# Optimization experiments

Hardware: AMD Instinct MI355X
Metric: run time of the kernel (lower is better)

The kernel has to match this reference:

```python
import jax, jax.numpy as jnp
import numpy as np
import math

D_MODEL = 1024
NUM_HEADS = 16
D_K = D_MODEL // NUM_HEADS
B, S = 2, 2048


def setup_inputs() -> dict:
    key = jax.random.key(0)
    ks = jax.random.split(key, 11)
    scale = 1.0 / math.sqrt(D_MODEL)
    inp = {
        "query": jax.random.normal(ks[0], (B, S, D_MODEL), jnp.float32),
        "key": jax.random.normal(ks[1], (B, S, D_MODEL), jnp.float32),
        "value": jax.random.normal(ks[2], (B, S, D_MODEL), jnp.float32),
        "Wq": jax.random.normal(ks[3], (D_MODEL, D_MODEL), jnp.float32) * scale,
        "bq": jnp.zeros((D_MODEL,), jnp.float32),
        "Wk": jax.random.normal(ks[4], (D_MODEL, D_MODEL), jnp.float32) * scale,
        "bk": jnp.zeros((D_MODEL,), jnp.float32),
        "Wv": jax.random.normal(ks[5], (D_MODEL, D_MODEL), jnp.float32) * scale,
        "bv": jnp.zeros((D_MODEL,), jnp.float32),
        "Wo": jax.random.normal(ks[6], (D_MODEL, D_MODEL), jnp.float32) * scale,
        "bo": jnp.zeros((D_MODEL,), jnp.float32),
    }
    return inp


def reference(query, key, value, Wq, bq, Wk, bk, Wv, bv, Wo, bo):
    b, s, _ = query.shape
    # QKV projections (torch Linear: x @ W.T + b)
    Q = query @ Wq.T + bq
    K = key @ Wk.T + bk
    V = value @ Wv.T + bv
    # [b, h, s, d_k]
    Q = Q.reshape(b, s, NUM_HEADS, D_K).transpose(0, 2, 1, 3)
    K = K.reshape(b, s, NUM_HEADS, D_K).transpose(0, 2, 1, 3)
    V = V.reshape(b, s, NUM_HEADS, D_K).transpose(0, 2, 1, 3)
    score = jnp.einsum("bhqd,bhkd->bhqk", Q, K) / math.sqrt(D_K)
    attn = jax.nn.softmax(score, axis=-1)
    out = jnp.einsum("bhqk,bhkd->bhqd", attn, V)
    out = out.transpose(0, 2, 1, 3).reshape(b, s, D_MODEL)
    return out @ Wo.T + bo
```

## Files before the change

kernel.cpp:

```cpp
#include <hip/hip_runtime.h>

#define NHEADS 16
#define SEQ    2048
#define BATCH  2
#define DMODEL 1024
#define MTOT   4096

typedef __attribute__((ext_vector_type(8)))  short short8;
typedef __attribute__((ext_vector_type(4)))  float f32x4;
typedef __attribute__((ext_vector_type(16))) float f32x16;

__device__ __forceinline__ unsigned short f32_to_bf16_rn(float x) {
  unsigned int u = __float_as_uint(x);
  u += 0x7fffu + ((u >> 16) & 1u);
  return (unsigned short)(u >> 16);
}

__device__ __forceinline__ unsigned cvt_pk_bf16(float lo, float hi_) {
  unsigned r;
  asm("v_cvt_pk_bf16_f32 %0, %1, %2" : "=v"(r) : "v"(lo), "v"(hi_));
  return r;
}

__device__ __forceinline__ void permlane32_swap(unsigned &a, unsigned &b) {
  asm("v_permlane32_swap_b32 %0, %1" : "+v"(a), "+v"(b));
}

__device__ __forceinline__ void async16(void* lds, const void* g) {
  __builtin_amdgcn_global_load_lds((const __attribute__((address_space(1))) unsigned int*)g,
                                   (__attribute__((address_space(3))) unsigned int*)lds, 16, 0, 0);
}

__global__ void cvt_bf16_kernel(const float* __restrict__ x0, const float* __restrict__ x1,
                                const float* __restrict__ x2,
                                const float* __restrict__ w0, const float* __restrict__ w1,
                                const float* __restrict__ w2, const float* __restrict__ w3,
                                unsigned short* __restrict__ obase)
{
  const int e = (blockIdx.x*256 + threadIdx.x)*8;
  const float* src;
  int local;
  if (e < 3*4194304) {
    const int t = e >> 22;
    src = t==0 ? x0 : t==1 ? x1 : x2;
    local = e & (4194304-1);
    src += local;
    local += t << 22;
  } else {
    const int f = e - 3*4194304;
    const int t = f >> 20;
    src = t==0 ? w0 : t==1 ? w1 : t==2 ? w2 : w3;
    src += (f & (1048576-1));
    local = e;
  }
  const float4 v0 = *(const float4*)(src);
  const float4 v1 = *(const float4*)(src + 4);
  union { unsigned short u[8]; uint4 v; } r;
  r.u[0] = f32_to_bf16_rn(v0.x); r.u[1] = f32_to_bf16_rn(v0.y);
  r.u[2] = f32_to_bf16_rn(v0.z); r.u[3] = f32_to_bf16_rn(v0.w);
  r.u[4] = f32_to_bf16_rn(v1.x); r.u[5] = f32_to_bf16_rn(v1.y);
  r.u[6] = f32_to_bf16_rn(v1.z); r.u[7] = f32_to_bf16_rn(v1.w);
  *(uint4*)(obase + local) = r.v;
}

template<int BM>
__device__ __forceinline__ void gemm_core(const unsigned short* __restrict__ A,
                                          const unsigned short* __restrict__ W,
                                          unsigned short* sA, unsigned short* sB,
                                          int m0, int n0, f32x4 (&acc)[BM/32][4])
{
  constexpr int MI = BM/32;
  const int t = threadIdx.x;
  const int lane = t & 63;
  const int wv = t >> 6;
  const int wm = wv >> 1, wn = wv & 1;
  const int lr = lane & 15, lk = lane >> 4;

  for (int kt = 0; kt < DMODEL/64; ++kt) {
    #pragma unroll
    for (int g = 0; g < MI; ++g) {
      const int o  = g*4096 + t*16;
      const int so = o ^ (((o >> 7) & 7) << 4);
      const int row = so >> 7, colE = (so & 127) >> 1;
      async16((char*)sA + o, A + (size_t)(m0 + row)*DMODEL + kt*64 + colE);
    }
    #pragma unroll
    for (int g = 0; g < 4; ++g) {
      const int o  = g*4096 + t*16;
      const int so = o ^ (((o >> 7) & 7) << 4);
      const int row = so >> 7, colE = (so & 127) >> 1;
      async16((char*)sB + o, W + (size_t)(n0 + row)*DMODEL + kt*64 + colE);
    }
    __syncthreads();
    #pragma unroll
    for (int ks = 0; ks < 2; ++ks) {
      short8 af[MI], bf[4];
      #pragma unroll
      for (int mi = 0; mi < MI; ++mi) {
        const int row = wm*(BM/2) + mi*16 + lr;
        const int sl  = (ks*4 + lk) ^ (row & 7);
        af[mi] = *(const short8*)(sA + row*64 + sl*8);
      }
      #pragma unroll
      for (int ni = 0; ni < 4; ++ni) {
        const int row = wn*64 + ni*16 + lr;
        const int sl  = (ks*4 + lk) ^ (row & 7);
        bf[ni] = *(const short8*)(sB + row*64 + sl*8);
      }
      #pragma unroll
      for (int mi = 0; mi < MI; ++mi)
        #pragma unroll
        for (int ni = 0; ni < 4; ++ni)
          acc[mi][ni] = __builtin_amdgcn_mfma_f32_16x16x32_bf16(af[mi], bf[ni], acc[mi][ni], 0, 0, 0);
    }
    __syncthreads();
  }
}

__global__ __launch_bounds__(256, 3)
void qkv_gemm_kernel(const unsigned short* __restrict__ Xq, const unsigned short* __restrict__ Xk,
                     const unsigned short* __restrict__ Xv,
                     const unsigned short* __restrict__ Wq, const unsigned short* __restrict__ Wk,
                     const unsigned short* __restrict__ Wv,
                     const float* __restrict__ bq, const float* __restrict__ bk,
                     const float* __restrict__ bv,
                     unsigned short* __restrict__ Qp, unsigned short* __restrict__ Kp,
                     unsigned short* __restrict__ Vtp)
{
  constexpr int BM = 128;
  constexpr int MI = BM/32;
  __shared__ __align__(16) unsigned short smem[17024];
  unsigned short* sA = smem;
  unsigned short* sB = smem + 8192;

  const int m0   = blockIdx.x * BM;
  const int nabs = blockIdx.y * 128;
  const int wsel = nabs >> 10;
  const int n0   = nabs & 1023;
  const unsigned short* A = wsel==0 ? Xq : wsel==1 ? Xk : Xv;
  const unsigned short* W = wsel==0 ? Wq : wsel==1 ? Wk : Wv;
  const float* bias       = wsel==0 ? bq : wsel==1 ? bk : bv;

  f32x4 acc[MI][4];
  #pragma unroll
  for (int mi = 0; mi < MI; ++mi)
    #pragma unroll
    for (int ni = 0; ni < 4; ++ni)
      acc[mi][ni] = {0.f, 0.f, 0.f, 0.f};

  gemm_core<BM>(A, W, sA, sB, m0, n0, acc);

  const int t = threadIdx.x, lane = t & 63, wvx = t >> 6;
  const int wm = wvx >> 1, wn = wvx & 1;
  const int lr = lane & 15, lk = lane >> 4;

  if (wsel == 2) {
    #pragma unroll
    for (int ni = 0; ni < 4; ++ni) {
      const float badd = bias[n0 + wn*64 + ni*16 + lr];
      #pragma unroll
      for (int mi = 0; mi < MI; ++mi)
        #pragma unroll
        for (int r = 0; r < 4; ++r) {
          const int ml = wm*(BM/2) + mi*16 + lk*4 + r;
          smem[(wn*64 + ni*16 + lr)*132 + ml] = f32_to_bf16_rn(acc[mi][ni][r] + badd);
        }
    }
    __syncthreads();
    const int bb = m0 >> 11, s0 = m0 & 2047;
    const int jr = (t & 15)*8, nr = t >> 4;
    #pragma unroll
    for (int pass = 0; pass < 8; ++pass) {
      const int n  = pass*16 + nr;
      const int nn = n0 + n, hh = nn >> 6, d = nn & 63;
      const short8 v = *(const short8*)(smem + n*132 + jr);
      *(short8*)(Vtp + (((size_t)bb*NHEADS + hh)*64 + d)*SEQ + s0 + jr) = v;
    }
  } else {
    unsigned short* dst = wsel==0 ? Qp : Kp;
    const float qscale = (wsel == 0) ? 0.125f * 1.4426950408889634f : 1.0f;
    #pragma unroll
    for (int ni = 0; ni < 4; ++ni) {
      const int nn = n0 + wn*64 + ni*16 + lr;
      const float badd = bias[nn];
      const int hh = nn >> 6, d = nn & 63;
      #pragma unroll
      for (int mi = 0; mi < MI; ++mi) {
        #pragma unroll
        for (int r = 0; r < 4; ++r) {
          const int m = m0 + wm*(BM/2) + mi*16 + lk*4 + r;
          const int bb = m >> 11, s = m & 2047;
          const float v = (acc[mi][ni][r] + badd) * qscale;
          dst[(((size_t)bb*NHEADS + hh)*SEQ + s)*64 + d] = f32_to_bf16_rn(v);
        }
      }
    }
  }
}

__global__ __launch_bounds__(256, 4)
void attn_kernel(const unsigned short* __restrict__ Qp, const unsigned short* __restrict__ Kp,
                 const unsigned short* __restrict__ Vtp,
                 unsigned short* __restrict__ Opar, float* __restrict__ Lpar)
{
  __shared__ __align__(16) unsigned short sm[16384];
  constexpr int NT = 1024/64;

  const int t = threadIdx.x, lane = t & 63, w = t >> 6;
  const int lq = lane & 31, hi = lane >> 5;
  const int f   = blockIdx.x;
  const int wid = (f & 7)*128 + (f >> 3);
  const int qt = wid & 15, h = (wid >> 4) & 15, b = (wid >> 8) & 1, half = wid >> 9;

  const size_t bh = (size_t)b*NHEADS + h;
  const unsigned short* Qh = Qp  + bh*SEQ*64;
  const unsigned short* Kh = Kp  + bh*SEQ*64 + (size_t)half*1024*64;
  const unsigned short* Vh = Vtp + bh*64*SEQ;
  const int q0 = qt*128 + w*32;

  const int stag = f & 3;
  for (int i = 0; i < stag; ++i) {
    __builtin_amdgcn_s_sleep(15);
    __builtin_amdgcn_s_sleep(15);
  }

  short8 qf[4];
  #pragma unroll
  for (int ks = 0; ks < 4; ++ks)
    qf[ks] = *(const short8*)(Qh + (size_t)(q0 + lq)*64 + ks*16 + hi*8);

  const unsigned short* srcp0;
  size_t sstride;
  if (w < 2) { srcp0 = Kh + (size_t)(w*32 + lq)*64 + hi*8;                      sstride = 64*64; }
  else       { srcp0 = Vh + (size_t)((w-2)*32 + lq)*2048 + half*1024 + hi*8;    sstride = 64;    }

  #pragma unroll
  for (int i = 0; i < 4; ++i)
    async16((char*)sm + w*4096 + i*1024, srcp0 + i*16);

  f32x16 o[2];
  float lsa[4] = {0.f, 0.f, 0.f, 0.f};
  #pragma unroll
  for (int d = 0; d < 2; ++d)
    #pragma unroll
    for (int r = 0; r < 16; ++r) o[d][r] = 0.f;

  #pragma unroll 2
  for (int kt = 0; kt < NT; ++kt) {
    {
      const unsigned short* sp = srcp0 + (size_t)((kt + 1) & (NT - 1))*sstride;
      const int nb = ((kt + 1) & 1) * 16384;
      #pragma unroll
      for (int i = 0; i < 4; ++i)
        async16((char*)sm + nb + w*4096 + i*1024, sp + i*16);
    }
    asm volatile("s_waitcnt vmcnt(4)" ::: "memory");
    __builtin_amdgcn_s_barrier();

    const unsigned short* base  = sm + (kt & 1)*8192;
    const unsigned short* vbase = base + 4096;

    f32x16 st[2];
    #pragma unroll
    for (int s = 0; s < 2; ++s)
      #pragma unroll
      for (int r = 0; r < 16; ++r) st[s][r] = 0.f;
    __builtin_amdgcn_s_setprio(1);
    #pragma unroll
    for (int sub = 0; sub < 2; ++sub)
      #pragma unroll
      for (int ks = 0; ks < 4; ++ks) {
        const short8 kf = *(const short8*)(base + (sub*4 + ks)*512 + lane*8);
        st[sub] = __builtin_amdgcn_mfma_f32_32x32x16_bf16(kf, qf[ks], st[sub], 0, 0, 0);
      }
    __builtin_amdgcn_s_setprio(0);

    #pragma unroll
    for (int s = 0; s < 2; ++s)
      #pragma unroll
      for (int r = 0; r < 16; ++r) {
        const float p = __builtin_amdgcn_exp2f(st[s][r]);
        st[s][r] = p;
        lsa[r & 3] += p;
      }

    #pragma unroll
    for (int sub = 0; sub < 2; ++sub) {
      union { unsigned u[4]; short8 s; } pA, pB;
      {
        unsigned x0 = cvt_pk_bf16(st[sub][0],  st[sub][1]);
        unsigned x1 = cvt_pk_bf16(st[sub][2],  st[sub][3]);
        unsigned y0 = cvt_pk_bf16(st[sub][4],  st[sub][5]);
        unsigned y1 = cvt_pk_bf16(st[sub][6],  st[sub][7]);
        permlane32_swap(x0, y0);
        permlane32_swap(x1, y1);
        pA.u[0] = x0; pA.u[1] = x1; pA.u[2] = y0; pA.u[3] = y1;
        unsigned z0 = cvt_pk_bf16(st[sub][8],  st[sub][9]);
        unsigned z1 = cvt_pk_bf16(st[sub][10], st[sub][11]);
        unsigned w0 = cvt_pk_bf16(st[sub][12], st[sub][13]);
        unsigned w1 = cvt_pk_bf16(st[sub][14], st[sub][15]);
        permlane32_swap(z0, w0);
        permlane32_swap(z1, w1);
        pB.u[0] = z0; pB.u[1] = z1; pB.u[2] = w0; pB.u[3] = w1;
      }
      const short8 v00 = *(const short8*)(vbase + (0*4 + 2*sub    )*512 + lane*8);
      const short8 v01 = *(const short8*)(vbase + (0*4 + 2*sub + 1)*512 + lane*8);
      const short8 v10 = *(const short8*)(vbase + (1*4 + 2*sub    )*512 + lane*8);
      const short8 v11 = *(const short8*)(vbase + (1*4 + 2*sub + 1)*512 + lane*8);
      __builtin_amdgcn_s_setprio(1);
      o[0] = __builtin_amdgcn_mfma_f32_32x32x16_bf16(v00, pA.s, o[0], 0, 0, 0);
      o[1] = __builtin_amdgcn_mfma_f32_32x32x16_bf16(v10, pA.s, o[1], 0, 0, 0);
      o[0] = __builtin_amdgcn_mfma_f32_32x32x16_bf16(v01, pB.s, o[0], 0, 0, 0);
      o[1] = __builtin_amdgcn_mfma_f32_32x32x16_bf16(v11, pB.s, o[1], 0, 0, 0);
      __builtin_amdgcn_s_setprio(0);
    }
    asm volatile("" ::: "memory");
    __builtin_amdgcn_s_barrier();
  }

  float lsum = (lsa[0] + lsa[1]) + (lsa[2] + lsa[3]);
  lsum += __shfl_xor(lsum, 32);
  if (lane < 32)
    Lpar[half*65536 + b*32768 + h*2048 + q0 + lq] = lsum;

  const size_t row = (size_t)b*SEQ + q0 + lq;
  unsigned short* orow = Opar + ((size_t)half*MTOT + row)*DMODEL + h*64;
  #pragma unroll
  for (int dblk = 0; dblk < 2; ++dblk)
    #pragma unroll
    for (int g = 0; g < 4; ++g) {
      union { unsigned short us[4]; uint2 v; } pk;
      #pragma unroll
      for (int r = 0; r < 4; ++r) pk.us[r] = f32_to_bf16_rn(o[dblk][g*4 + r]);
      *(uint2*)(orow + dblk*32 + g*8 + hi*4) = pk.v;
    }
}

__global__ void combine_kernel(const unsigned short* __restrict__ Opar,
                               const float* __restrict__ Lpar,
                               unsigned short* __restrict__ Op)
{
  const int flat = blockIdx.x*256 + threadIdx.x;
  const int row  = flat >> 8;
  const int col4 = flat & 255;
  const int b = row >> 11, q = row & 2047, h = col4 >> 4;

  const uint2 a = *(const uint2*)(Opar + (size_t)row*DMODEL + col4*4);
  const uint2 c = *(const uint2*)(Opar + (size_t)(MTOT + row)*DMODEL + col4*4);
  const float l0 = Lpar[b*32768 + h*2048 + q];
  const float l1 = Lpar[65536 + b*32768 + h*2048 + q];
  const float inv = __builtin_amdgcn_rcpf(l0 + l1);

  union { unsigned u[2]; uint2 v; } ua, uc;
  ua.v = a; uc.v = c;
  union { unsigned short us[4]; uint2 v; } out;
  #pragma unroll
  for (int j = 0; j < 4; ++j) {
    const unsigned va = ((j & 1) ? (ua.u[j >> 1] >> 16) : (ua.u[j >> 1] & 0xffffu)) << 16;
    const unsigned vc = ((j & 1) ? (uc.u[j >> 1] >> 16) : (uc.u[j >> 1] & 0xffffu)) << 16;
    const float s = (__uint_as_float(va) + __uint_as_float(vc)) * inv;
    out.us[j] = f32_to_bf16_rn(s);
  }
  *(uint2*)(Op + (size_t)row*DMODEL + col4*4) = out.v;
}

__global__ __launch_bounds__(256, 2)
void oproj_gemm_kernel(const unsigned short* __restrict__ Oin, const unsigned short* __restrict__ Wo,
                       const float* __restrict__ bo, float* __restrict__ out)
{
  constexpr int BM = 64;
  constexpr int MI = BM/32;
  __shared__ __align__(16) unsigned short sA[BM*64];
  __shared__ __align__(16) unsigned short sB[128*64];
  const int m0 = blockIdx.x * BM;
  const int n0 = blockIdx.y * 128;

  f32x4 acc[MI][4];
  #pragma unroll
  for (int mi = 0; mi < MI; ++mi)
    #pragma unroll
    for (int ni = 0; ni < 4; ++ni)
      acc[mi][ni] = {0.f,0.f,0.f,0.f};

  gemm_core<BM>(Oin, Wo, sA, sB, m0, n0, acc);

  const int t = threadIdx.x, lane = t & 63, wvx = t >> 6;
  const int wm = wvx >> 1, wn = wvx & 1;
  const int lr = lane & 15, lk = lane >> 4;

  #pragma unroll
  for (int ni = 0; ni < 4; ++ni) {
    const int nn = n0 + wn*64 + ni*16 + lr;
    const float badd = bo[nn];
    #pragma unroll
    for (int mi = 0; mi < MI; ++mi)
      #pragma unroll
      for (int r = 0; r < 4; ++r) {
        const int m = m0 + wm*(BM/2) + mi*16 + lk*4 + r;
        out[(size_t)m*DMODEL + nn] = acc[mi][ni][r] + badd;
      }
  }
}

extern "C" void kernel_launch(void* const* d_in, const int* in_sizes, int n_in,
                              void* d_out, int out_size, void* d_ws, size_t ws_size,
                              hipStream_t stream) {
  const float* query = (const float*)d_in[0];
  const float* key   = (const float*)d_in[1];
  const float* value = (const float*)d_in[2];
  const float* Wq    = (const float*)d_in[3];
  const float* bq    = (const float*)d_in[4];
  const float* Wk    = (const float*)d_in[5];
  const float* bk    = (const float*)d_in[6];
  const float* Wv    = (const float*)d_in[7];
  const float* bv    = (const float*)d_in[8];
  const float* Wo    = (const float*)d_in[9];
  const float* bo    = (const float*)d_in[10];

  const size_t NX = (size_t)MTOT*DMODEL;
  const size_t NW = (size_t)DMODEL*DMODEL;
  unsigned short* w   = (unsigned short*)d_ws;
  unsigned short* Xq  = w;
  unsigned short* Xk  = Xq  + NX;
  unsigned short* Xv  = Xk  + NX;
  unsigned short* Wqp = Xv  + NX;
  unsigned short* Wkp = Wqp + NW;
  unsigned short* Wvp = Wkp + NW;
  unsigned short* Wop = Wvp + NW;
  unsigned short* Qp  = Wop + NW;
  unsigned short* Kp  = Qp  + NX;
  unsigned short* Vtp = Kp  + NX;
  unsigned short* Opb = Vtp + NX;
  unsigned short* Opar = w;
  float*          Lpar = (float*)(w + 2*NX);

  cvt_bf16_kernel<<<dim3(8192), 256, 0, stream>>>(
      query, key, value, Wq, Wk, Wv, Wo, w);
  qkv_gemm_kernel<<<dim3(32, 24), 256, 0, stream>>>(
      Xq, Xk, Xv, Wqp, Wkp, Wvp, bq, bk, bv, Qp, Kp, Vtp);
  attn_kernel<<<dim3(1024), 256, 0, stream>>>(Qp, Kp, Vtp, Opar, Lpar);
  combine_kernel<<<dim3(4096), 256, 0, stream>>>(Opar, Lpar, Opb);
  oproj_gemm_kernel<<<dim3(64, 8), 256, 0, stream>>>(Opb, Wop, bo, (float*)d_out);
}
```

Baseline: 122.5 us.

## Process two 32-row query sub-tiles per wave to reuse K/V LDS tiles

Each wave now handles 64 query rows (two 32-row halves) instead of 32, so every K and V fragment read from LDS feeds two MFMAs. The grid is halved to 512 blocks, launch bounds drop to 2 blocks per CU, and the s_sleep start stagger and the zeroing of score accumulators are removed (the first MFMA now takes a zero input). This cuts LDS traffic and global K/V loads per unit of work, at the cost of more registers, lower occupancy and fewer blocks to spread across CUs.

```diff
diff --git a/kernel.cpp b/kernel.cpp
--- a/kernel.cpp
+++ b/kernel.cpp
@@ -198,7 +198,7 @@
   }
 }
 
-__global__ __launch_bounds__(256, 4)
+__global__ __launch_bounds__(256, 2)
 void attn_kernel(const unsigned short* __restrict__ Qp, const unsigned short* __restrict__ Kp,
                  const unsigned short* __restrict__ Vtp,
                  unsigned short* __restrict__ Opar, float* __restrict__ Lpar)
@@ -209,25 +209,25 @@
   const int t = threadIdx.x, lane = t & 63, w = t >> 6;
   const int lq = lane & 31, hi = lane >> 5;
   const int f   = blockIdx.x;
-  const int wid = (f & 7)*128 + (f >> 3);
-  const int qt = wid & 15, h = (wid >> 4) & 15, b = (wid >> 8) & 1, half = wid >> 9;
+  const int wid = (f & 7)*64 + (f >> 3);
+  const int qt = wid & 7, h = (wid >> 3) & 15, b = (wid >> 7) & 1, half = (wid >> 8) & 1;
 
   const size_t bh = (size_t)b*NHEADS + h;
   const unsigned short* Qh = Qp  + bh*SEQ*64;
   const unsigned short* Kh = Kp  + bh*SEQ*64 + (size_t)half*1024*64;
   const unsigned short* Vh = Vtp + bh*64*SEQ;
-  const int q0 = qt*128 + w*32;
-
-  const int stag = f & 3;
-  for (int i = 0; i < stag; ++i) {
-    __builtin_amdgcn_s_sleep(15);
-    __builtin_amdgcn_s_sleep(15);
-  }
-
-  short8 qf[4];
-  #pragma unroll
-  for (int ks = 0; ks < 4; ++ks)
-    qf[ks] = *(const short8*)(Qh + (size_t)(q0 + lq)*64 + ks*16 + hi*8);
+  const int q0 = qt*256 + w*64;
+
+  short8 qf[2][4];
+  #pragma unroll
+  for (int qh = 0; qh < 2; ++qh)
+    #pragma unroll
+    for (int ks = 0; ks < 4; ++ks)
+      qf[qh][ks] = *(const short8*)(Qh + (size_t)(q0 + qh*32 + lq)*64 + ks*16 + hi*8);
+
+  f32x16 z16;
+  #pragma unroll
+  for (int r = 0; r < 16; ++r) z16[r] = 0.f;
 
   const unsigned short* srcp0;
   size_t sstride;
@@ -238,14 +238,18 @@
   for (int i = 0; i < 4; ++i)
     async16((char*)sm + w*4096 + i*1024, srcp0 + i*16);
 
-  f32x16 o[2];
-  float lsa[4] = {0.f, 0.f, 0.f, 0.f};
-  #pragma unroll
-  for (int d = 0; d < 2; ++d)
-    #pragma unroll
-    for (int r = 0; r < 16; ++r) o[d][r] = 0.f;
-
-  #pragma unroll 2
+  f32x16 o[2][2];
+  float lsa[2][4];
+  #pragma unroll
+  for (int qh = 0; qh < 2; ++qh) {
+    #pragma unroll
+    for (int d = 0; d < 2; ++d)
+      #pragma unroll
+      for (int r = 0; r < 16; ++r) o[qh][d][r] = 0.f;
+    #pragma unroll
+    for (int j = 0; j < 4; ++j) lsa[qh][j] = 0.f;
+  }
+
   for (int kt = 0; kt < NT; ++kt) {
     {
       const unsigned short* sp = srcp0 + (size_t)((kt + 1) & (NT - 1))*sstride;
@@ -260,80 +264,101 @@
     const unsigned short* base  = sm + (kt & 1)*8192;
     const unsigned short* vbase = base + 4096;
 
-    f32x16 st[2];
-    #pragma unroll
-    for (int s = 0; s < 2; ++s)
-      #pragma unroll
-      for (int r = 0; r < 16; ++r) st[s][r] = 0.f;
+    f32x16 st[2][2];
     __builtin_amdgcn_s_setprio(1);
     #pragma unroll
-    for (int sub = 0; sub < 2; ++sub)
+    for (int sub = 0; sub < 2; ++sub) {
       #pragma unroll
       for (int ks = 0; ks < 4; ++ks) {
         const short8 kf = *(const short8*)(base + (sub*4 + ks)*512 + lane*8);
-        st[sub] = __builtin_amdgcn_mfma_f32_32x32x16_bf16(kf, qf[ks], st[sub], 0, 0, 0);
-      }
+        if (ks == 0) {
+          st[0][sub] = __builtin_amdgcn_mfma_f32_32x32x16_bf16(kf, qf[0][0], z16, 0, 0, 0);
+          st[1][sub] = __builtin_amdgcn_mfma_f32_32x32x16_bf16(kf, qf[1][0], z16, 0, 0, 0);
+        } else {
+          st[0][sub] = __builtin_amdgcn_mfma_f32_32x32x16_bf16(kf, qf[0][ks], st[0][sub], 0, 0, 0);
+          st[1][sub] = __builtin_amdgcn_mfma_f32_32x32x16_bf16(kf, qf[1][ks], st[1][sub], 0, 0, 0);
+        }
+      }
+    }
     __builtin_amdgcn_s_setprio(0);
 
-    #pragma unroll
-    for (int s = 0; s < 2; ++s)
-      #pragma unroll
-      for (int r = 0; r < 16; ++r) {
-        const float p = __builtin_amdgcn_exp2f(st[s][r]);
-        st[s][r] = p;
-        lsa[r & 3] += p;
-      }
-
-    #pragma unroll
-    for (int sub = 0; sub < 2; ++sub) {
-      union { unsigned u[4]; short8 s; } pA, pB;
-      {
-        unsigned x0 = cvt_pk_bf16(st[sub][0],  st[sub][1]);
-        unsigned x1 = cvt_pk_bf16(st[sub][2],  st[sub][3]);
-        unsigned y0 = cvt_pk_bf16(st[sub][4],  st[sub][5]);
-        unsigned y1 = cvt_pk_bf16(st[sub][6],  st[sub][7]);
+    unsigned pw[2][2][8];
+    #pragma unroll
+    for (int qh = 0; qh < 2; ++qh)
+      #pragma unroll
+      for (int sub = 0; sub < 2; ++sub) {
+        #pragma unroll
+        for (int r = 0; r < 16; ++r) {
+          const float p = __builtin_amdgcn_exp2f(st[qh][sub][r]);
+          st[qh][sub][r] = p;
+          lsa[qh][r & 3] += p;
+        }
+        unsigned x0 = cvt_pk_bf16(st[qh][sub][0],  st[qh][sub][1]);
+        unsigned x1 = cvt_pk_bf16(st[qh][sub][2],  st[qh][sub][3]);
+        unsigned y0 = cvt_pk_bf16(st[qh][sub][4],  st[qh][sub][5]);
+        unsigned y1 = cvt_pk_bf16(st[qh][sub][6],  st[qh][sub][7]);
         permlane32_swap(x0, y0);
         permlane32_swap(x1, y1);
-        pA.u[0] = x0; pA.u[1] = x1; pA.u[2] = y0; pA.u[3] = y1;
-        unsigned z0 = cvt_pk_bf16(st[sub][8],  st[sub][9]);
-        unsigned z1 = cvt_pk_bf16(st[sub][10], st[sub][11]);
-        unsigned w0 = cvt_pk_bf16(st[sub][12], st[sub][13]);
-        unsigned w1 = cvt_pk_bf16(st[sub][14], st[sub][15]);
+        pw[qh][sub][0] = x0; pw[qh][sub][1] = x1; pw[qh][sub][2] = y0; pw[qh][sub][3] = y1;
+        unsigned z0 = cvt_pk_bf16(st[qh][sub][8],  st[qh][sub][9]);
+        unsigned z1 = cvt_pk_bf16(st[qh][sub][10], st[qh][sub][11]);
+        unsigned w0 = cvt_pk_bf16(st[qh][sub][12], st[qh][sub][13]);
+        unsigned w1 = cvt_pk_bf16(st[qh][sub][14], st[qh][sub][15]);
         permlane32_swap(z0, w0);
         permlane32_swap(z1, w1);
-        pB.u[0] = z0; pB.u[1] = z1; pB.u[2] = w0; pB.u[3] = w1;
-      }
+        pw[qh][sub][4] = z0; pw[qh][sub][5] = z1; pw[qh][sub][6] = w0; pw[qh][sub][7] = w1;
+      }
+
+    #pragma unroll
+    for (int sub = 0; sub < 2; ++sub) {
       const short8 v00 = *(const short8*)(vbase + (0*4 + 2*sub    )*512 + lane*8);
       const short8 v01 = *(const short8*)(vbase + (0*4 + 2*sub + 1)*512 + lane*8);
       const short8 v10 = *(const short8*)(vbase + (1*4 + 2*sub    )*512 + lane*8);
       const short8 v11 = *(const short8*)(vbase + (1*4 + 2*sub + 1)*512 + lane*8);
       __builtin_amdgcn_s_setprio(1);
-      o[0] = __builtin_amdgcn_mfma_f32_32x32x16_bf16(v00, pA.s, o[0], 0, 0, 0);
-      o[1] = __builtin_amdgcn_mfma_f32_32x32x16_bf16(v10, pA.s, o[1], 0, 0, 0);
-      o[0] = __builtin_amdgcn_mfma_f32_32x32x16_bf16(v01, pB.s, o[0], 0, 0, 0);
-      o[1] = __builtin_amdgcn_mfma_f32_32x32x16_bf16(v11, pB.s, o[1], 0, 0, 0);
+      #pragma unroll
+      for (int qh = 0; qh < 2; ++qh) {
+        union { unsigned u[4]; short8 s; } pA, pB;
+        pA.u[0] = pw[qh][sub][0]; pA.u[1] = pw[qh][sub][1];
+        pA.u[2] = pw[qh][sub][2]; pA.u[3] = pw[qh][sub][3];
+        pB.u[0] = pw[qh][sub][4]; pB.u[1] = pw[qh][sub][5];
+        pB.u[2] = pw[qh][sub][6]; pB.u[3] = pw[qh][sub][7];
+        o[qh][0] = __builtin_amdgcn_mfma_f32_32x32x16_bf16(v00, pA.s, o[qh][0], 0, 0, 0);
+        o[qh][1] = __builtin_amdgcn_mfma_f32_32x32x16_bf16(v10, pA.s, o[qh][1], 0, 0, 0);
+        o[qh][0] = __builtin_amdgcn_mfma_f32_32x32x16_bf16(v01, pB.s, o[qh][0], 0, 0, 0);
+        o[qh][1] = __builtin_amdgcn_mfma_f32_32x32x16_bf16(v11, pB.s, o[qh][1], 0, 0, 0);
+      }
       __builtin_amdgcn_s_setprio(0);
     }
     asm volatile("" ::: "memory");
     __builtin_amdgcn_s_barrier();
   }
 
-  float lsum = (lsa[0] + lsa[1]) + (lsa[2] + lsa[3]);
-  lsum += __shfl_xor(lsum, 32);
-  if (lane < 32)
-    Lpar[half*65536 + b*32768 + h*2048 + q0 + lq] = lsum;
-
-  const size_t row = (size_t)b*SEQ + q0 + lq;
-  unsigned short* orow = Opar + ((size_t)half*MTOT + row)*DMODEL + h*64;
-  #pragma unroll
-  for (int dblk = 0; dblk < 2; ++dblk)
-    #pragma unroll
-    for (int g = 0; g < 4; ++g) {
-      union { unsigned short us[4]; uint2 v; } pk;
-      #pragma unroll
-      for (int r = 0; r < 4; ++r) pk.us[r] = f32_to_bf16_rn(o[dblk][g*4 + r]);
-      *(uint2*)(orow + dblk*32 + g*8 + hi*4) = pk.v;
-    }
+  float lsum[2];
+  #pragma unroll
+  for (int qh = 0; qh < 2; ++qh) {
+    lsum[qh] = (lsa[qh][0] + lsa[qh][1]) + (lsa[qh][2] + lsa[qh][3]);
+    lsum[qh] += __shfl_xor(lsum[qh], 32);
+  }
+  if (lane < 32) {
+    Lpar[half*65536 + b*32768 + h*2048 + q0 + lq]      = lsum[0];
+    Lpar[half*65536 + b*32768 + h*2048 + q0 + 32 + lq] = lsum[1];
+  }
+
+  #pragma unroll
+  for (int qh = 0; qh < 2; ++qh) {
+    const size_t row = (size_t)b*SEQ + q0 + qh*32 + lq;
+    unsigned short* orow = Opar + ((size_t)half*MTOT + row)*DMODEL + h*64;
+    #pragma unroll
+    for (int dblk = 0; dblk < 2; ++dblk)
+      #pragma unroll
+      for (int g = 0; g < 4; ++g) {
+        union { unsigned short us[4]; uint2 v; } pk;
+        #pragma unroll
+        for (int r = 0; r < 4; ++r) pk.us[r] = f32_to_bf16_rn(o[qh][dblk][g*4 + r]);
+        *(uint2*)(orow + dblk*32 + g*8 + hi*4) = pk.v;
+      }
+  }
 }
 
 __global__ void combine_kernel(const unsigned short* __restrict__ Opar,
@@ -438,7 +463,7 @@
       query, key, value, Wq, Wk, Wv, Wo, w);
   qkv_gemm_kernel<<<dim3(32, 24), 256, 0, stream>>>(
       Xq, Xk, Xv, Wqp, Wkp, Wvp, bq, bk, bv, Qp, Kp, Vtp);
-  attn_kernel<<<dim3(1024), 256, 0, stream>>>(Qp, Kp, Vtp, Opar, Lpar);
+  attn_kernel<<<dim3(512), 256, 0, stream>>>(Qp, Kp, Vtp, Opar, Lpar);
   combine_kernel<<<dim3(4096), 256, 0, stream>>>(Opar, Lpar, Opb);
   oproj_gemm_kernel<<<dim3(64, 8), 256, 0, stream>>>(Opb, Wop, bo, (float*)d_out);
 }
```

Measured after the change: 118.1 us. 3.6% less time.

## Drop split-KV attention and combine kernel; each block processes full key range

Applied to the files above, without the earlier changes.

Removes the two-way key split in the attention kernel so each block iterates over all 2048 keys and normalizes its output directly, eliminating the separate combine kernel and the partial output/sum buffers. The grid halves to 512 blocks and launch bounds drop to 2 blocks per SM. It also removes the startup sleep staggering and the setprio hints, zero-initializes the score MFMA via a constant zero operand, and groups the exp/convert work before the PV MFMAs. The trade is fewer blocks (less parallelism and latency hiding) against saving a kernel launch plus the partial-result memory traffic.

```diff
diff --git a/kernel.cpp b/kernel.cpp
--- a/kernel.cpp
+++ b/kernel.cpp
@@ -198,41 +198,38 @@
   }
 }
 
-__global__ __launch_bounds__(256, 4)
+__global__ __launch_bounds__(256, 2)
 void attn_kernel(const unsigned short* __restrict__ Qp, const unsigned short* __restrict__ Kp,
-                 const unsigned short* __restrict__ Vtp,
-                 unsigned short* __restrict__ Opar, float* __restrict__ Lpar)
+                 const unsigned short* __restrict__ Vtp, unsigned short* __restrict__ Op)
 {
   __shared__ __align__(16) unsigned short sm[16384];
-  constexpr int NT = 1024/64;
+  constexpr int NT = SEQ/64;
 
   const int t = threadIdx.x, lane = t & 63, w = t >> 6;
   const int lq = lane & 31, hi = lane >> 5;
   const int f   = blockIdx.x;
-  const int wid = (f & 7)*128 + (f >> 3);
-  const int qt = wid & 15, h = (wid >> 4) & 15, b = (wid >> 8) & 1, half = wid >> 9;
+  const int wid = (f & 7)*64 + (f >> 3);
+  const int qt = wid & 15, h = (wid >> 4) & 15, b = wid >> 8;
 
   const size_t bh = (size_t)b*NHEADS + h;
   const unsigned short* Qh = Qp  + bh*SEQ*64;
-  const unsigned short* Kh = Kp  + bh*SEQ*64 + (size_t)half*1024*64;
+  const unsigned short* Kh = Kp  + bh*SEQ*64;
   const unsigned short* Vh = Vtp + bh*64*SEQ;
   const int q0 = qt*128 + w*32;
 
-  const int stag = f & 3;
-  for (int i = 0; i < stag; ++i) {
-    __builtin_amdgcn_s_sleep(15);
-    __builtin_amdgcn_s_sleep(15);
-  }
-
   short8 qf[4];
   #pragma unroll
   for (int ks = 0; ks < 4; ++ks)
     qf[ks] = *(const short8*)(Qh + (size_t)(q0 + lq)*64 + ks*16 + hi*8);
 
+  f32x16 z16;
+  #pragma unroll
+  for (int r = 0; r < 16; ++r) z16[r] = 0.f;
+
   const unsigned short* srcp0;
   size_t sstride;
-  if (w < 2) { srcp0 = Kh + (size_t)(w*32 + lq)*64 + hi*8;                      sstride = 64*64; }
-  else       { srcp0 = Vh + (size_t)((w-2)*32 + lq)*2048 + half*1024 + hi*8;    sstride = 64;    }
+  if (w < 2) { srcp0 = Kh + (size_t)(w*32 + lq)*64 + hi*8;       sstride = 64*64; }
+  else       { srcp0 = Vh + (size_t)((w-2)*32 + lq)*2048 + hi*8; sstride = 64;    }
 
   #pragma unroll
   for (int i = 0; i < 4; ++i)
@@ -245,7 +242,6 @@
     #pragma unroll
     for (int r = 0; r < 16; ++r) o[d][r] = 0.f;
 
-  #pragma unroll 2
   for (int kt = 0; kt < NT; ++kt) {
     {
       const unsigned short* sp = srcp0 + (size_t)((kt + 1) & (NT - 1))*sstride;
@@ -262,57 +258,55 @@
 
     f32x16 st[2];
     #pragma unroll
-    for (int s = 0; s < 2; ++s)
-      #pragma unroll
-      for (int r = 0; r < 16; ++r) st[s][r] = 0.f;
-    __builtin_amdgcn_s_setprio(1);
-    #pragma unroll
-    for (int sub = 0; sub < 2; ++sub)
+    for (int sub = 0; sub < 2; ++sub) {
       #pragma unroll
       for (int ks = 0; ks < 4; ++ks) {
         const short8 kf = *(const short8*)(base + (sub*4 + ks)*512 + lane*8);
-        st[sub] = __builtin_amdgcn_mfma_f32_32x32x16_bf16(kf, qf[ks], st[sub], 0, 0, 0);
-      }
-    __builtin_amdgcn_s_setprio(0);
-
-    #pragma unroll
-    for (int s = 0; s < 2; ++s)
+        if (ks == 0)
+          st[sub] = __builtin_amdgcn_mfma_f32_32x32x16_bf16(kf, qf[0], z16, 0, 0, 0);
+        else
+          st[sub] = __builtin_amdgcn_mfma_f32_32x32x16_bf16(kf, qf[ks], st[sub], 0, 0, 0);
+      }
+    }
+
+    unsigned pw[2][8];
+    #pragma unroll
+    for (int sub = 0; sub < 2; ++sub) {
       #pragma unroll
       for (int r = 0; r < 16; ++r) {
-        const float p = __builtin_amdgcn_exp2f(st[s][r]);
-        st[s][r] = p;
+        const float p = __builtin_amdgcn_exp2f(st[sub][r]);
+        st[sub][r] = p;
         lsa[r & 3] += p;
       }
+      unsigned x0 = cvt_pk_bf16(st[sub][0],  st[sub][1]);
+      unsigned x1 = cvt_pk_bf16(st[sub][2],  st[sub][3]);
+      unsigned y0 = cvt_pk_bf16(st[sub][4],  st[sub][5]);
+      unsigned y1 = cvt_pk_bf16(st[sub][6],  st[sub][7]);
+      permlane32_swap(x0, y0);
+      permlane32_swap(x1, y1);
+      pw[sub][0] = x0; pw[sub][1] = x1; pw[sub][2] = y0; pw[sub][3] = y1;
+      unsigned z0 = cvt_pk_bf16(st[sub][8],  st[sub][9]);
+      unsigned z1 = cvt_pk_bf16(st[sub][10], st[sub][11]);
+      unsigned w0 = cvt_pk_bf16(st[sub][12], st[sub][13]);
+      unsigned w1 = cvt_pk_bf16(st[sub][14], st[sub][15]);
+      permlane32_swap(z0, w0);
+      permlane32_swap(z1, w1);
+      pw[sub][4] = z0; pw[sub][5] = z1; pw[sub][6] = w0; pw[sub][7] = w1;
+    }
 
     #pragma unroll
     for (int sub = 0; sub < 2; ++sub) {
-      union { unsigned u[4]; short8 s; } pA, pB;
-      {
-        unsigned x0 = cvt_pk_bf16(st[sub][0],  st[sub][1]);
-        unsigned x1 = cvt_pk_bf16(st[sub][2],  st[sub][3]);
-        unsigned y0 = cvt_pk_bf16(st[sub][4],  st[sub][5]);
-        unsigned y1 = cvt_pk_bf16(st[sub][6],  st[sub][7]);
-        permlane32_swap(x0, y0);
-        permlane32_swap(x1, y1);
-        pA.u[0] = x0; pA.u[1] = x1; pA.u[2] = y0; pA.u[3] = y1;
-        unsigned z0 = cvt_pk_bf16(st[sub][8],  st[sub][9]);
-        unsigned z1 = cvt_pk_bf16(st[sub][10], st[sub][11]);
-        unsigned w0 = cvt_pk_bf16(st[sub][12], st[sub][13]);
-        unsigned w1 = cvt_pk_bf16(st[sub][14], st[sub][15]);
-        permlane32_swap(z0, w0);
-        permlane32_swap(z1, w1);
-        pB.u[0] = z0; pB.u[1] = z1; pB.u[2] = w0; pB.u[3] = w1;
-      }
       const short8 v00 = *(const short8*)(vbase + (0*4 + 2*sub    )*512 + lane*8);
       const short8 v01 = *(const short8*)(vbase + (0*4 + 2*sub + 1)*512 + lane*8);
       const short8 v10 = *(const short8*)(vbase + (1*4 + 2*sub    )*512 + lane*8);
       const short8 v11 = *(const short8*)(vbase + (1*4 + 2*sub + 1)*512 + lane*8);
-      __builtin_amdgcn_s_setprio(1);
+      union { unsigned u[4]; short8 s; } pA, pB;
+      pA.u[0] = pw[sub][0]; pA.u[1] = pw[sub][1]; pA.u[2] = pw[sub][2]; pA.u[3] = pw[sub][3];
+      pB.u[0] = pw[sub][4]; pB.u[1] = pw[sub][5]; pB.u[2] = pw[sub][6]; pB.u[3] = pw[sub][7];
       o[0] = __builtin_amdgcn_mfma_f32_32x32x16_bf16(v00, pA.s, o[0], 0, 0, 0);
       o[1] = __builtin_amdgcn_mfma_f32_32x32x16_bf16(v10, pA.s, o[1], 0, 0, 0);
       o[0] = __builtin_amdgcn_mfma_f32_32x32x16_bf16(v01, pB.s, o[0], 0, 0, 0);
       o[1] = __builtin_amdgcn_mfma_f32_32x32x16_bf16(v11, pB.s, o[1], 0, 0, 0);
-      __builtin_amdgcn_s_setprio(0);
     }
     asm volatile("" ::: "memory");
     __builtin_amdgcn_s_barrier();
@@ -320,48 +314,17 @@
 
   float lsum = (lsa[0] + lsa[1]) + (lsa[2] + lsa[3]);
   lsum += __shfl_xor(lsum, 32);
-  if (lane < 32)
-    Lpar[half*65536 + b*32768 + h*2048 + q0 + lq] = lsum;
-
-  const size_t row = (size_t)b*SEQ + q0 + lq;
-  unsigned short* orow = Opar + ((size_t)half*MTOT + row)*DMODEL + h*64;
+  const float inv = __builtin_amdgcn_rcpf(lsum);
+  unsigned short* orow = Op + ((size_t)b*SEQ + q0 + lq)*DMODEL + h*64;
   #pragma unroll
   for (int dblk = 0; dblk < 2; ++dblk)
     #pragma unroll
     for (int g = 0; g < 4; ++g) {
       union { unsigned short us[4]; uint2 v; } pk;
       #pragma unroll
-      for (int r = 0; r < 4; ++r) pk.us[r] = f32_to_bf16_rn(o[dblk][g*4 + r]);
+      for (int r = 0; r < 4; ++r) pk.us[r] = f32_to_bf16_rn(o[dblk][g*4 + r] * inv);
       *(uint2*)(orow + dblk*32 + g*8 + hi*4) = pk.v;
     }
-}
-
-__global__ void combine_kernel(const unsigned short* __restrict__ Opar,
-                               const float* __restrict__ Lpar,
-                               unsigned short* __restrict__ Op)
-{
-  const int flat = blockIdx.x*256 + threadIdx.x;
-  const int row  = flat >> 8;
-  const int col4 = flat & 255;
-  const int b = row >> 11, q = row & 2047, h = col4 >> 4;
-
-  const uint2 a = *(const uint2*)(Opar + (size_t)row*DMODEL + col4*4);
-  const uint2 c = *(const uint2*)(Opar + (size_t)(MTOT + row)*DMODEL + col4*4);
-  const float l0 = Lpar[b*32768 + h*2048 + q];
-  const float l1 = Lpar[65536 + b*32768 + h*2048 + q];
-  const float inv = __builtin_amdgcn_rcpf(l0 + l1);
-
-  union { unsigned u[2]; uint2 v; } ua, uc;
-  ua.v = a; uc.v = c;
-  union { unsigned short us[4]; uint2 v; } out;
-  #pragma unroll
-  for (int j = 0; j < 4; ++j) {
-    const unsigned va = ((j & 1) ? (ua.u[j >> 1] >> 16) : (ua.u[j >> 1] & 0xffffu)) << 16;
-    const unsigned vc = ((j & 1) ? (uc.u[j >> 1] >> 16) : (uc.u[j >> 1] & 0xffffu)) << 16;
-    const float s = (__uint_as_float(va) + __uint_as_float(vc)) * inv;
-    out.us[j] = f32_to_bf16_rn(s);
-  }
-  *(uint2*)(Op + (size_t)row*DMODEL + col4*4) = out.v;
 }
 
 __global__ __launch_bounds__(256, 2)
@@ -431,14 +394,11 @@
   unsigned short* Kp  = Qp  + NX;
   unsigned short* Vtp = Kp  + NX;
   unsigned short* Opb = Vtp + NX;
-  unsigned short* Opar = w;
-  float*          Lpar = (float*)(w + 2*NX);
 
   cvt_bf16_kernel<<<dim3(8192), 256, 0, stream>>>(
       query, key, value, Wq, Wk, Wv, Wo, w);
   qkv_gemm_kernel<<<dim3(32, 24), 256, 0, stream>>>(
       Xq, Xk, Xv, Wqp, Wkp, Wvp, bq, bk, bv, Qp, Kp, Vtp);
-  attn_kernel<<<dim3(1024), 256, 0, stream>>>(Qp, Kp, Vtp, Opar, Lpar);
-  combine_kernel<<<dim3(4096), 256, 0, stream>>>(Opar, Lpar, Opb);
+  attn_kernel<<<dim3(512), 256, 0, stream>>>(Qp, Kp, Vtp, Opb);
   oproj_gemm_kernel<<<dim3(64, 8), 256, 0, stream>>>(Opb, Wop, bo, (float*)d_out);
 }
```

After: 109.9 us. 10.3% less time.
